# Kernel tuning notes

Measured on AMD Instinct MI355X. Metric: run time of the kernel, lower is better.

The kernel has to match this reference:

```python
import jax, jax.numpy as jnp
import numpy as np

HEADS = 16
DIM_HEAD = 64
EPS = 1e-8


def setup_inputs() -> dict:
    key = jax.random.key(0)
    ks = jax.random.split(key, 5)
    B, N, D = 2, 2048, 1024
    inner = HEADS * DIM_HEAD
    return {
        "x": jax.random.normal(ks[0], (B, N, D), jnp.float32),
        "Wq": jax.random.normal(ks[1], (D, inner), jnp.float32) * (D ** -0.5),
        "Wkv": jax.random.normal(ks[2], (D, 2 * inner), jnp.float32) * (D ** -0.5),
        "Wo": jax.random.normal(ks[3], (inner, D), jnp.float32) * (inner ** -0.5),
        "bo": jax.random.normal(ks[4], (D,), jnp.float32) * 0.02,
    }


def reference(x, Wq, Wkv, Wo, bo):
    # Self-attention (context = x), causal, memory-efficient path.
    # The chunked online-softmax in the source is mathematically equivalent to:
    #   gm = rowwise max of raw (unmasked) scores (stop-gradient, as in .detach())
    #   p  = exp(s - gm) with causal-masked entries zeroed (exp(-finfo.max) == 0)
    #   out = (p @ v) / (sum_j p + eps)
    B, N, D = x.shape
    H, Dh = HEADS, DIM_HEAD
    scale = Dh ** -0.5

    q = (x @ Wq).reshape(B, N, H, Dh).transpose(0, 2, 1, 3)  # b h n d
    kv = x @ Wkv
    k = kv[..., : H * Dh].reshape(B, N, H, Dh).transpose(0, 2, 1, 3)
    v = kv[..., H * Dh :].reshape(B, N, H, Dh).transpose(0, 2, 1, 3)

    s = jnp.einsum("bhid,bhjd->bhij", q * scale, k)  # b h i j
    gm = jax.lax.stop_gradient(jnp.max(s, axis=-1, keepdims=True))
    causal_mask = jnp.triu(jnp.ones((N, N), bool), 1)  # True above diagonal -> masked
    p = jnp.where(causal_mask, 0.0, jnp.exp(s - gm))
    num = jnp.einsum("bhij,bhjd->bhid", p, v)
    out = num / (jnp.sum(p, axis=-1, keepdims=True) + EPS)  # b h n d

    out = out.transpose(0, 2, 1, 3).reshape(B, N, H * Dh)  # b n (h d)
    return out @ Wo + bo
```

## Files before the change

### kernel.cpp

```cpp
#include <hip/hip_runtime.h>

typedef _Float16 f16;
typedef __attribute__((ext_vector_type(8))) _Float16 f16x8;
typedef __attribute__((ext_vector_type(4))) _Float16 f16x4;
typedef __attribute__((ext_vector_type(4))) float   f32x4;

typedef unsigned int u32;
typedef __attribute__((address_space(1))) const u32 gu32;
typedef __attribute__((address_space(3))) u32 lu32;

__device__ inline void gll16(const void* g, void* l) {
  __builtin_amdgcn_global_load_lds((gu32*)g, (lu32*)l, 16, 0, 0);
}

__global__ void prep(const float* __restrict__ Wq, const float* __restrict__ Wkv,
                     const float* __restrict__ Wo, const float* __restrict__ x,
                     f16* __restrict__ WqkvT, f16* __restrict__ WoT, f16* __restrict__ xb) {
  __shared__ float tile[32][33];
  int z = blockIdx.z;
  int tx = threadIdx.x, ty = threadIdx.y;
  if (z == 3) {
    size_t flat = ((size_t)(blockIdx.y * 64 + blockIdx.x) * 256 + ty * 32 + tx) * 2;
    for (int i = 0; i < 2; i++) {
      float4 v = ((const float4*)x)[flat + i];
      f16x4 r = { (f16)v.x, (f16)v.y, (f16)v.z, (f16)v.w };
      ((f16x4*)xb)[flat + i] = r;
    }
    return;
  }
  const float* src; f16* dst; int W;
  if (z == 0)      { src = Wq;  dst = WqkvT;                       W = 1024; }
  else if (z == 1) { src = Wkv; dst = WqkvT + (size_t)1024 * 1024; W = 2048; }
  else             { src = Wo;  dst = WoT;                         W = 1024; }
  int c0 = blockIdx.x * 32, r0 = blockIdx.y * 32;
  if (c0 >= W) return;
  for (int i = 0; i < 4; i++)
    tile[ty + i * 8][tx] = src[(size_t)(r0 + ty + i * 8) * W + c0 + tx];
  __syncthreads();
  for (int i = 0; i < 4; i++)
    dst[(size_t)(c0 + ty + i * 8) * 1024 + r0 + tx] = (f16)tile[tx][ty + i * 8];
}

__global__ __launch_bounds__(256) void gemm1(
    const f16* __restrict__ A, const f16* __restrict__ Bt,
    f16* __restrict__ qb, f16* __restrict__ kb, f16* __restrict__ vtb) {
  const int K = 1024;
  __shared__ f16 As[128 * 32];
  __shared__ f16 Bs[128 * 32];
  int tid = threadIdx.x;
  int wave = tid >> 6, lane = tid & 63, quad = lane >> 4, l16 = lane & 15;
  int m0 = blockIdx.y * 128, n0 = blockIdx.x * 128;
  int wr = (wave >> 1) * 64, wc = (wave & 1) * 64;

  f32x4 acc[4][4] = {};

  int gA = (((lane & 3) ^ ((lane >> 3) & 3))) * 8;
  const f16* Ag = A  + (size_t)(m0 + wave * 32 + (lane >> 2)) * K + gA;
  const f16* Bg = Bt + (size_t)(n0 + wave * 32 + (lane >> 2)) * K + gA;
  f16* Asw = As + wave * 1024;
  f16* Bsw = Bs + wave * 1024;
  int rsz = (l16 >> 1) & 3;

  for (int k0 = 0; k0 < K; k0 += 32) {
    gll16(Ag + k0, Asw);
    gll16(Ag + (size_t)16 * K + k0, Asw + 512);
    gll16(Bg + k0, Bsw);
    gll16(Bg + (size_t)16 * K + k0, Bsw + 512);
    __syncthreads();
    f16x8 af[4], bf[4];
    for (int mt = 0; mt < 4; mt++)
      af[mt] = *(const f16x8*)&As[(wr + mt * 16 + l16) * 32 + ((quad ^ rsz) << 3)];
    for (int nt = 0; nt < 4; nt++)
      bf[nt] = *(const f16x8*)&Bs[(wc + nt * 16 + l16) * 32 + ((quad ^ rsz) << 3)];
    for (int mt = 0; mt < 4; mt++)
      for (int nt = 0; nt < 4; nt++)
        acc[mt][nt] = __builtin_amdgcn_mfma_f32_16x16x32_f16(af[mt], bf[nt], acc[mt][nt], 0, 0, 0);
    __syncthreads();
  }

  if (n0 < 2048) {
    for (int mt = 0; mt < 4; mt++)
      for (int nt = 0; nt < 4; nt++)
        for (int r = 0; r < 4; r++) {
          int row = m0 + wr + mt * 16 + quad * 4 + r;
          int col = n0 + wc + nt * 16 + l16;
          float v = acc[mt][nt][r];
          int b = row >> 11, n = row & 2047;
          if (col < 1024) {
            qb[(((size_t)b * 16 + (col >> 6)) * 2048 + n) * 64 + (col & 63)] =
                (f16)(v * 0.1803368801111137f);
          } else {
            int c = col - 1024;
            kb[(((size_t)b * 16 + (c >> 6)) * 2048 + n) * 64 + (c & 63)] = (f16)v;
          }
        }
  } else {
    for (int mt = 0; mt < 4; mt++)
      for (int nt = 0; nt < 4; nt++) {
        int rb = m0 + wr + mt * 16 + quad * 4;
        int c  = n0 + wc + nt * 16 + l16 - 2048;
        int b = rb >> 11, n = rb & 2047;
        f16x4 pk = { (f16)acc[mt][nt][0], (f16)acc[mt][nt][1],
                     (f16)acc[mt][nt][2], (f16)acc[mt][nt][3] };
        size_t idx = (((size_t)(b * 16 + (c >> 6)) * 32 + (n >> 6)) * 64 + (c & 63)) * 64 + (n & 63);
        *(f16x4*)&vtb[idx] = pk;
      }
  }
}

__global__ __launch_bounds__(256) void gemm2(
    const f16* __restrict__ A, const f16* __restrict__ Bt,
    const float* __restrict__ bo, float* __restrict__ outf) {
  const int K = 1024;
  __shared__ f16 As[128 * 32];
  __shared__ f16 Bs[64 * 32];
  int tid = threadIdx.x;
  int wave = tid >> 6, lane = tid & 63, quad = lane >> 4, l16 = lane & 15;
  int m0 = blockIdx.y * 128, n0 = blockIdx.x * 64;
  int wr = (wave >> 1) * 64, wc = (wave & 1) * 32;

  f32x4 acc[4][2] = {};

  int gA = (((lane & 3) ^ ((lane >> 3) & 3))) * 8;
  const f16* Ag = A  + (size_t)(m0 + wave * 32 + (lane >> 2)) * K + gA;
  const f16* Bg = Bt + (size_t)(n0 + wave * 16 + (lane >> 2)) * K + gA;
  f16* Asw = As + wave * 1024;
  f16* Bsw = Bs + wave * 512;
  int rsz = (l16 >> 1) & 3;

  for (int k0 = 0; k0 < K; k0 += 32) {
    gll16(Ag + k0, Asw);
    gll16(Ag + (size_t)16 * K + k0, Asw + 512);
    gll16(Bg + k0, Bsw);
    __syncthreads();
    f16x8 af[4], bf[2];
    for (int mt = 0; mt < 4; mt++)
      af[mt] = *(const f16x8*)&As[(wr + mt * 16 + l16) * 32 + ((quad ^ rsz) << 3)];
    for (int nt = 0; nt < 2; nt++)
      bf[nt] = *(const f16x8*)&Bs[(wc + nt * 16 + l16) * 32 + ((quad ^ rsz) << 3)];
    for (int mt = 0; mt < 4; mt++)
      for (int nt = 0; nt < 2; nt++)
        acc[mt][nt] = __builtin_amdgcn_mfma_f32_16x16x32_f16(af[mt], bf[nt], acc[mt][nt], 0, 0, 0);
    __syncthreads();
  }

  for (int mt = 0; mt < 4; mt++)
    for (int nt = 0; nt < 2; nt++)
      for (int r = 0; r < 4; r++) {
        int row = m0 + wr + mt * 16 + quad * 4 + r;
        int col = n0 + wc + nt * 16 + l16;
        outf[(size_t)row * 1024 + col] = acc[mt][nt][r] + bo[col];
      }
}

__global__ __launch_bounds__(256, 4) void attn(
    const f16* __restrict__ qb, const f16* __restrict__ kb,
    const f16* __restrict__ vtb, f16* __restrict__ ob) {
  __shared__ f16 Ks[2][64 * 64];
  __shared__ f16 Vs[2][64 * 64];
  __shared__ f16 Ps[4][16 * 64];
  int tid = threadIdx.x, wave = tid >> 6, lane = tid & 63, quad = lane >> 4, l16 = lane & 15;
  int l7 = l16 & 7;

  int bx = blockIdx.x;
  int q = bx >> 8, r = bx & 255;
  int xcd = r & 7, idx = r >> 3;
  int bh = xcd * 4 + (idx & 3);
  int srem = idx >> 2;
  int t = (q == 0) ? srem : (q == 1) ? 15 - srem : (q == 2) ? 16 + srem : 31 - srem;
  int qi0 = t * 64;
  int b = bh >> 4, h = bh & 15;

  const f16* Q  = qb + (size_t)bh * 2048 * 64;
  const char* Kg = (const char*)(kb + (size_t)bh * 2048 * 64);
  const char* Vbase = (const char*)(vtb + (size_t)bh * 32 * 4096);
  int wq0 = qi0 + wave * 16;
  int i = wq0 + l16;

  f16x8 qf[2];
  for (int ks = 0; ks < 2; ks++)
    qf[ks] = *(const f16x8*)&Q[(size_t)(wq0 + l16) * 64 + ks * 32 + quad * 8];

  f32x4 acc[4] = {};
  float lrow = 0.f;

  int sg = ((lane & 7) ^ ((lane >> 3) & 7)) * 16;
  int jl = wave * 16 + (lane >> 3);

  int end = qi0 + 64;

  gll16(Kg + (size_t)jl * 128 + sg,          (char*)&Ks[0][0] + wave * 2048);
  gll16(Kg + (size_t)(jl + 8) * 128 + sg,    (char*)&Ks[0][0] + wave * 2048 + 1024);
  gll16(Vbase + (size_t)jl * 128 + sg,       (char*)&Vs[0][0] + wave * 2048);
  gll16(Vbase + (size_t)(jl + 8) * 128 + sg, (char*)&Vs[0][0] + wave * 2048 + 1024);
  __syncthreads();

  int cur = 0;
  for (int j0 = 0; j0 < end; j0 += 64) {
    if (j0 + 64 < end) {
      const char* kg = Kg + (size_t)(j0 + 64) * 128;
      const char* vt = Vbase + (size_t)((j0 + 64) >> 6) * 8192;
      char* kd = (char*)&Ks[cur ^ 1][0] + wave * 2048;
      char* vd = (char*)&Vs[cur ^ 1][0] + wave * 2048;
      gll16(kg + (size_t)jl * 128 + sg,       kd);
      gll16(kg + (size_t)(jl + 8) * 128 + sg, kd + 1024);
      gll16(vt + (size_t)jl * 128 + sg,       vd);
      gll16(vt + (size_t)(jl + 8) * 128 + sg, vd + 1024);
    }

    {
      const f16* KsC = &Ks[cur][0];
      const f16* VsC = &Vs[cur][0];
      f16x8 kf[4][2], vf[4][2];
      for (int nt = 0; nt < 4; nt++)
        for (int ks = 0; ks < 2; ks++) {
          int pos = ((ks * 4 + quad) ^ l7) << 3;
          kf[nt][ks] = *(const f16x8*)&KsC[(nt * 16 + l16) * 64 + pos];
          vf[nt][ks] = *(const f16x8*)&VsC[(nt * 16 + l16) * 64 + pos];
        }

      f32x4 st[4];
      for (int nt = 0; nt < 4; nt++) {
        f32x4 z = {0.f, 0.f, 0.f, 0.f};
        z = __builtin_amdgcn_mfma_f32_16x16x32_f16(kf[nt][0], qf[0], z, 0, 0, 0);
        z = __builtin_amdgcn_mfma_f32_16x16x32_f16(kf[nt][1], qf[1], z, 0, 0, 0);
        st[nt] = z;
      }
      if (j0 + 63 > wq0) {
        for (int nt = 0; nt < 4; nt++) {
          int jc = j0 + nt * 16 + quad * 4;
          for (int rr = 0; rr < 4; rr++)
            st[nt][rr] = (jc + rr <= i) ? st[nt][rr] : -1e30f;
        }
      }
      float psum = 0.f;
      for (int nt = 0; nt < 4; nt++) {
        f16x4 pk;
        for (int rr = 0; rr < 4; rr++) {
          float p = __builtin_amdgcn_exp2f(st[nt][rr] - 14.426950408889634f);
          psum += p;
          pk[rr] = (f16)p;
        }
        int pos = (nt * 2 + (quad >> 1)) ^ l7;
        *(f16x4*)((char*)&Ps[wave][0] + l16 * 128 + pos * 16 + (quad & 1) * 8) = pk;
      }
      psum += __shfl_xor(psum, 16);
      psum += __shfl_xor(psum, 32);
      lrow += psum;

      for (int ks = 0; ks < 2; ks++) {
        f16x8 pf = *(const f16x8*)((char*)&Ps[wave][0] + l16 * 128 + (((ks * 4 + quad) ^ l7) * 16));
        for (int nt = 0; nt < 4; nt++)
          acc[nt] = __builtin_amdgcn_mfma_f32_16x16x32_f16(vf[nt][ks], pf, acc[nt], 0, 0, 0);
      }
    }
    __syncthreads();
    cur ^= 1;
  }

  float inv = 1.f / (lrow + 1e-8f);
  int n = wq0 + l16;
  for (int nt = 0; nt < 4; nt++) {
    f16x4 o = { (f16)(acc[nt][0] * inv), (f16)(acc[nt][1] * inv),
                (f16)(acc[nt][2] * inv), (f16)(acc[nt][3] * inv) };
    *(f16x4*)&ob[((size_t)b * 2048 + n) * 1024 + h * 64 + nt * 16 + quad * 4] = o;
  }
}

extern "C" void kernel_launch(void* const* d_in, const int* in_sizes, int n_in,
                              void* d_out, int out_size, void* d_ws, size_t ws_size,
                              hipStream_t stream) {
  const float* x   = (const float*)d_in[0];
  const float* Wq  = (const float*)d_in[1];
  const float* Wkv = (const float*)d_in[2];
  const float* Wo  = (const float*)d_in[3];
  const float* bo  = (const float*)d_in[4];
  float* out = (float*)d_out;

  char* ws = (char*)d_ws;
  f16* xb    = (f16*)ws;  ws += (size_t)4096 * 1024 * 2;
  f16* WqkvT = (f16*)ws;  ws += (size_t)3072 * 1024 * 2;
  f16* WoT   = (f16*)ws;  ws += (size_t)1024 * 1024 * 2;
  f16* qb    = (f16*)ws;  ws += (size_t)32 * 2048 * 64 * 2;
  f16* kb    = (f16*)ws;  ws += (size_t)32 * 2048 * 64 * 2;
  f16* vtb   = (f16*)ws;  ws += (size_t)32 * 64 * 2048 * 2;
  f16* ob    = xb;

  prep<<<dim3(64, 32, 4), dim3(32, 8), 0, stream>>>(Wq, Wkv, Wo, x, WqkvT, WoT, xb);
  gemm1<<<dim3(24, 32), 256, 0, stream>>>(xb, WqkvT, qb, kb, vtb);
  attn<<<dim3(1024), 256, 0, stream>>>(qb, kb, vtb, ob);
  gemm2<<<dim3(16, 32), 256, 0, stream>>>(ob, WoT, bo, out);
}
```

Before: 174.9 us.

## Triple-buffer LDS in projection GEMMs with prefetch two k-steps ahead

Both projection GEMMs move from a single LDS buffer with load-then-sync to a three-stage ring. Direct-to-LDS global loads are issued two k-tiles ahead, and explicit vmcnt waits plus one barrier per iteration replace the two __syncthreads. The goal is to overlap global memory latency with MFMA work. In exchange it triples LDS use per block, which may lower occupancy, and it depends on hand-counted vmcnt values being correct.

After: 177.2 us. About the same (+1.3%).

```diff
diff --git a/kernel.cpp b/kernel.cpp
--- a/kernel.cpp
+++ b/kernel.cpp
@@ -45,8 +45,8 @@
     const f16* __restrict__ A, const f16* __restrict__ Bt,
     f16* __restrict__ qb, f16* __restrict__ kb, f16* __restrict__ vtb) {
   const int K = 1024;
-  __shared__ f16 As[128 * 32];
-  __shared__ f16 Bs[128 * 32];
+  __shared__ f16 As[3][128 * 32];
+  __shared__ f16 Bs[3][128 * 32];
   int tid = threadIdx.x;
   int wave = tid >> 6, lane = tid & 63, quad = lane >> 4, l16 = lane & 15;
   int m0 = blockIdx.y * 128, n0 = blockIdx.x * 128;
@@ -57,25 +57,46 @@
   int gA = (((lane & 3) ^ ((lane >> 3) & 3))) * 8;
   const f16* Ag = A  + (size_t)(m0 + wave * 32 + (lane >> 2)) * K + gA;
   const f16* Bg = Bt + (size_t)(n0 + wave * 32 + (lane >> 2)) * K + gA;
-  f16* Asw = As + wave * 1024;
-  f16* Bsw = Bs + wave * 1024;
   int rsz = (l16 >> 1) & 3;
 
+  for (int t = 0; t < 2; t++) {
+    f16* Asw = &As[t][0] + wave * 1024;
+    f16* Bsw = &Bs[t][0] + wave * 1024;
+    gll16(Ag + t * 32, Asw);
+    gll16(Ag + (size_t)16 * K + t * 32, Asw + 512);
+    gll16(Bg + t * 32, Bsw);
+    gll16(Bg + (size_t)16 * K + t * 32, Bsw + 512);
+  }
+  asm volatile("s_waitcnt vmcnt(4)" ::: "memory");
+  __builtin_amdgcn_s_barrier();
+  __builtin_amdgcn_sched_barrier(0);
+
+  int cb = 0;
   for (int k0 = 0; k0 < K; k0 += 32) {
-    gll16(Ag + k0, Asw);
-    gll16(Ag + (size_t)16 * K + k0, Asw + 512);
-    gll16(Bg + k0, Bsw);
-    gll16(Bg + (size_t)16 * K + k0, Bsw + 512);
-    __syncthreads();
+    if (k0 + 64 < K) {
+      int sb = cb + 2; if (sb >= 3) sb -= 3;
+      f16* Asw = &As[sb][0] + wave * 1024;
+      f16* Bsw = &Bs[sb][0] + wave * 1024;
+      gll16(Ag + k0 + 64, Asw);
+      gll16(Ag + (size_t)16 * K + k0 + 64, Asw + 512);
+      gll16(Bg + k0 + 64, Bsw);
+      gll16(Bg + (size_t)16 * K + k0 + 64, Bsw + 512);
+    }
+    const f16* Asr = &As[cb][0];
+    const f16* Bsr = &Bs[cb][0];
     f16x8 af[4], bf[4];
     for (int mt = 0; mt < 4; mt++)
-      af[mt] = *(const f16x8*)&As[(wr + mt * 16 + l16) * 32 + ((quad ^ rsz) << 3)];
+      af[mt] = *(const f16x8*)&Asr[(wr + mt * 16 + l16) * 32 + ((quad ^ rsz) << 3)];
     for (int nt = 0; nt < 4; nt++)
-      bf[nt] = *(const f16x8*)&Bs[(wc + nt * 16 + l16) * 32 + ((quad ^ rsz) << 3)];
+      bf[nt] = *(const f16x8*)&Bsr[(wc + nt * 16 + l16) * 32 + ((quad ^ rsz) << 3)];
     for (int mt = 0; mt < 4; mt++)
       for (int nt = 0; nt < 4; nt++)
         acc[mt][nt] = __builtin_amdgcn_mfma_f32_16x16x32_f16(af[mt], bf[nt], acc[mt][nt], 0, 0, 0);
-    __syncthreads();
+    if (k0 + 64 < K) asm volatile("s_waitcnt vmcnt(4)" ::: "memory");
+    else             asm volatile("s_waitcnt vmcnt(0)" ::: "memory");
+    __builtin_amdgcn_s_barrier();
+    __builtin_amdgcn_sched_barrier(0);
+    cb = (cb == 2) ? 0 : cb + 1;
   }
 
   if (n0 < 2048) {
@@ -112,8 +133,8 @@
     const f16* __restrict__ A, const f16* __restrict__ Bt,
     const float* __restrict__ bo, float* __restrict__ outf) {
   const int K = 1024;
-  __shared__ f16 As[128 * 32];
-  __shared__ f16 Bs[64 * 32];
+  __shared__ f16 As[3][128 * 32];
+  __shared__ f16 Bs[3][64 * 32];
   int tid = threadIdx.x;
   int wave = tid >> 6, lane = tid & 63, quad = lane >> 4, l16 = lane & 15;
   int m0 = blockIdx.y * 128, n0 = blockIdx.x * 64;
@@ -124,24 +145,44 @@
   int gA = (((lane & 3) ^ ((lane >> 3) & 3))) * 8;
   const f16* Ag = A  + (size_t)(m0 + wave * 32 + (lane >> 2)) * K + gA;
   const f16* Bg = Bt + (size_t)(n0 + wave * 16 + (lane >> 2)) * K + gA;
-  f16* Asw = As + wave * 1024;
-  f16* Bsw = Bs + wave * 512;
   int rsz = (l16 >> 1) & 3;
 
+  for (int t = 0; t < 2; t++) {
+    f16* Asw = &As[t][0] + wave * 1024;
+    f16* Bsw = &Bs[t][0] + wave * 512;
+    gll16(Ag + t * 32, Asw);
+    gll16(Ag + (size_t)16 * K + t * 32, Asw + 512);
+    gll16(Bg + t * 32, Bsw);
+  }
+  asm volatile("s_waitcnt vmcnt(3)" ::: "memory");
+  __builtin_amdgcn_s_barrier();
+  __builtin_amdgcn_sched_barrier(0);
+
+  int cb = 0;
   for (int k0 = 0; k0 < K; k0 += 32) {
-    gll16(Ag + k0, Asw);
-    gll16(Ag + (size_t)16 * K + k0, Asw + 512);
-    gll16(Bg + k0, Bsw);
-    __syncthreads();
+    if (k0 + 64 < K) {
+      int sb = cb + 2; if (sb >= 3) sb -= 3;
+      f16* Asw = &As[sb][0] + wave * 1024;
+      f16* Bsw = &Bs[sb][0] + wave * 512;
+      gll16(Ag + k0 + 64, Asw);
+      gll16(Ag + (size_t)16 * K + k0 + 64, Asw + 512);
+      gll16(Bg + k0 + 64, Bsw);
+    }
+    const f16* Asr = &As[cb][0];
+    const f16* Bsr = &Bs[cb][0];
     f16x8 af[4], bf[2];
     for (int mt = 0; mt < 4; mt++)
-      af[mt] = *(const f16x8*)&As[(wr + mt * 16 + l16) * 32 + ((quad ^ rsz) << 3)];
+      af[mt] = *(const f16x8*)&Asr[(wr + mt * 16 + l16) * 32 + ((quad ^ rsz) << 3)];
     for (int nt = 0; nt < 2; nt++)
-      bf[nt] = *(const f16x8*)&Bs[(wc + nt * 16 + l16) * 32 + ((quad ^ rsz) << 3)];
+      bf[nt] = *(const f16x8*)&Bsr[(wc + nt * 16 + l16) * 32 + ((quad ^ rsz) << 3)];
     for (int mt = 0; mt < 4; mt++)
       for (int nt = 0; nt < 2; nt++)
         acc[mt][nt] = __builtin_amdgcn_mfma_f32_16x16x32_f16(af[mt], bf[nt], acc[mt][nt], 0, 0, 0);
-    __syncthreads();
+    if (k0 + 64 < K) asm volatile("s_waitcnt vmcnt(3)" ::: "memory");
+    else             asm volatile("s_waitcnt vmcnt(0)" ::: "memory");
+    __builtin_amdgcn_s_barrier();
+    __builtin_amdgcn_sched_barrier(0);
+    cb = (cb == 2) ? 0 : cb + 1;
   }
 
   for (int mt = 0; mt < 4; mt++)
```
